# Kernel optimization log

Measured on AMD Instinct MI355X. Metric: run time of the kernel, lower is better.

Reference implementation:

```python
import math
import jax, jax.numpy as jnp
import numpy as np

B, T, C = 2, 2048, 1024
NH, D = 16, 64


def setup_inputs() -> dict:
    key = jax.random.key(0)
    k1, k2, k3, k4 = jax.random.split(key, 4)
    x = jax.random.normal(k1, (B, T, C), dtype=jnp.float32)
    W_attn = jax.random.normal(k2, (3 * C, C), dtype=jnp.float32) * 0.02
    b_attn = jnp.zeros((3 * C,), dtype=jnp.float32)
    W_proj = jax.random.normal(k3, (C, C), dtype=jnp.float32) * 0.02
    b_proj = jnp.zeros((C,), dtype=jnp.float32)
    bV = jax.random.normal(k4, (NH, D), dtype=jnp.float32) * 0.05
    return {"x": x, "W_attn": W_attn, "b_attn": b_attn,
            "W_proj": W_proj, "b_proj": b_proj, "bV": bV}


def reference(x, W_attn, b_attn, W_proj, b_proj, bV):
    Bb, Tt, Cc = x.shape
    # fused qkv projection (torch Linear: x @ W.T + b)
    qkv = x @ W_attn.T + b_attn                     # [B,T,3C]
    q, k, v = jnp.split(qkv, 3, axis=2)
    q = q.reshape(Bb, Tt, NH, D).transpose(0, 2, 1, 3)  # [B,H,T,D]
    k = k.reshape(Bb, Tt, NH, D).transpose(0, 2, 1, 3)
    v = v.reshape(Bb, Tt, NH, D).transpose(0, 2, 1, 3)
    v = v + bV[None, :, None, :]                    # V-O symmetry-breaking bias
    scores = jnp.einsum('bhqd,bhkd->bhqk', q, k) / math.sqrt(D)
    causal = jnp.tril(jnp.ones((Tt, Tt), dtype=bool))
    scores = jnp.where(causal[None, None], scores, -jnp.inf)
    att = jax.nn.softmax(scores, axis=-1)           # [B,H,T,T]
    y = jnp.einsum('bhqk,bhkd->bhqd', att, v)
    y = y.transpose(0, 2, 1, 3).reshape(Bb, Tt, Cc)
    return y @ W_proj.T + b_proj
```

## Files before the change

kernel.cpp:

```cpp
#include <hip/hip_runtime.h>

#define DEVI __device__ __forceinline__

typedef __bf16 bf16x8 __attribute__((ext_vector_type(8)));
typedef float  f32x4  __attribute__((ext_vector_type(4)));

static DEVI unsigned short f2bf(float f) {
  unsigned u = __builtin_bit_cast(unsigned, f);
  u = u + 0x7fffu + ((u >> 16) & 1u);
  return (unsigned short)(u >> 16);
}
static DEVI unsigned short f2bf_trunc(float f) {
  return (unsigned short)(__builtin_bit_cast(unsigned, f) >> 16);
}

#define EXP2F(x) __builtin_amdgcn_exp2f(x)

typedef __attribute__((address_space(3))) void* lds_vp;
typedef const __attribute__((address_space(1))) void* glob_vp;
#define GL2LDS16(g, l) __builtin_amdgcn_global_load_lds((glob_vp)(g), (lds_vp)(l), 16, 0, 0)

__global__ void __launch_bounds__(256) conv_bf16(const float* __restrict__ in,
                                                 unsigned short* __restrict__ out, int n4) {
  int i = (int)blockIdx.x * 256 + (int)threadIdx.x;
  if (i >= n4) return;
  float4 v = reinterpret_cast<const float4*>(in)[i];
  ushort4 o;
  o.x = f2bf(v.x); o.y = f2bf(v.y); o.z = f2bf(v.z); o.w = f2bf(v.w);
  reinterpret_cast<ushort4*>(out)[i] = o;
}

#define GSTAGE(t_, bufi_) do {                                                    \
    const int kk_ = (t_)*64;                                                      \
    _Pragma("unroll")                                                             \
    for (int jq = 0; jq < 4; jq++) {                                              \
      const int row_ = w*32 + jq*8 + (l >> 3);                                    \
      GL2LDS16(A  + (size_t)(r0 + row_)*K + kk_ + scol, &sA[bufi_][(w*32 + jq*8)*64]); \
      GL2LDS16(Bm + (size_t)(c0 + row_)*K + kk_ + scol, &sB[bufi_][(w*32 + jq*8)*64]); \
    } } while (0)

template<int EPI>
__global__ void __launch_bounds__(256) gemm_bt(
    const unsigned short* __restrict__ A,
    const unsigned short* __restrict__ Bm,
    const float* __restrict__ bias,
    const float* __restrict__ bV,
    unsigned short* __restrict__ outQ,
    unsigned short* __restrict__ outK,
    unsigned short* __restrict__ outVT,
    float* __restrict__ outF)
{
  constexpr int K = 1024;
  constexpr int NSTEP = 16;
  __shared__ unsigned short sA[2][128*64];
  __shared__ unsigned short sB[2][128*64];
  const int tid = (int)threadIdx.x;
  const int w = tid >> 6;
  const int l = tid & 63;
  const int l15 = l & 15, lg = l >> 4;
  const int r0 = (int)blockIdx.y * 128;
  const int c0 = (int)blockIdx.x * 128;
  const int wr = (w >> 1) * 64, wc = (w & 1) * 64;
  const int scol = ((l & 7) ^ (l >> 3)) * 8;
  const int rdsw = (l & 7) * 8;

  f32x4 acc[4][4];
#pragma unroll
  for (int i = 0; i < 4; i++)
#pragma unroll
    for (int j = 0; j < 4; j++) acc[i][j] = (f32x4){0.f, 0.f, 0.f, 0.f};

  GSTAGE(0, 0);
  GSTAGE(1, 1);
  for (int t = 0; t < NSTEP; t++) {
    if (t < NSTEP-1) asm volatile("s_waitcnt vmcnt(8)" ::: "memory");
    else             asm volatile("s_waitcnt vmcnt(0)" ::: "memory");
    __builtin_amdgcn_s_barrier();
    const int bufi = t & 1;
    bf16x8 av[2][4], bv[2][4];
#pragma unroll
    for (int ks = 0; ks < 2; ks++) {
#pragma unroll
      for (int mi = 0; mi < 4; mi++)
        av[ks][mi] = *(const bf16x8*)&sA[bufi][(wr + mi*16 + l15)*64 + ((ks*32 + lg*8) ^ rdsw)];
#pragma unroll
      for (int ni = 0; ni < 4; ni++)
        bv[ks][ni] = *(const bf16x8*)&sB[bufi][(wc + ni*16 + l15)*64 + ((ks*32 + lg*8) ^ rdsw)];
    }
    asm volatile("s_waitcnt lgkmcnt(0)" ::: "memory");
    __builtin_amdgcn_s_barrier();
    if (t + 2 < NSTEP) GSTAGE(t + 2, bufi);
#pragma unroll
    for (int ks = 0; ks < 2; ks++)
#pragma unroll
      for (int mi = 0; mi < 4; mi++)
#pragma unroll
        for (int ni = 0; ni < 4; ni++)
          acc[mi][ni] = __builtin_amdgcn_mfma_f32_16x16x32_bf16(av[ks][mi], bv[ks][ni], acc[mi][ni], 0, 0, 0);
  }

#pragma unroll
  for (int mi = 0; mi < 4; mi++) {
    const int rbase = r0 + wr + mi*16 + lg*4;
#pragma unroll
    for (int ni = 0; ni < 4; ni++) {
      const int c = c0 + wc + ni*16 + l15;
      const float bsv = bias[c];
      if constexpr (EPI == 0) {
        const int which = c >> 10;
        const int cc = c & 1023;
        const int h = cc >> 6;
        const int d = cc & 63;
        const float bvv = (which == 2) ? bV[h*64 + d] : 0.f;
#pragma unroll
        for (int i = 0; i < 4; i++) {
          const int rr = rbase + i;
          const int b = rr >> 11;
          const int t = rr & 2047;
          const int bh = b*16 + h;
          const float v = acc[mi][ni][i] + bsv;
          if (which == 0)      outQ[((size_t)bh*2048 + t)*64 + d] = f2bf(v * 0.1803368801f);
          else if (which == 1) outK[((size_t)bh*2048 + t)*64 + d] = f2bf(v);
          else                 outVT[((size_t)bh*64 + d)*2048 + t] = f2bf(v + bvv);
        }
      } else {
#pragma unroll
        for (int i = 0; i < 4; i++)
          outF[(size_t)(rbase + i)*1024 + c] = acc[mi][ni][i] + bsv;
      }
    }
  }
}

#define ASTAGE(kt_, bufi_) do {                                                   \
    _Pragma("unroll")                                                             \
    for (int jq = 0; jq < 2; jq++) {                                              \
      const int chunk_ = w*2 + jq;                                                \
      GL2LDS16(Kh + (size_t)((kt_)*64 + chunk_*8 + (l >> 3))*64 + srcsw, &sK[bufi_][chunk_*512]); \
      GL2LDS16(Vh + (size_t)(chunk_*8 + (l >> 3))*2048 + (kt_)*64 + srcsw, &sV[bufi_][chunk_*512]); \
    } } while (0)

__global__ void __launch_bounds__(256) attn_fwd(
    const unsigned short* __restrict__ Q,
    const unsigned short* __restrict__ Kc,
    const unsigned short* __restrict__ VT,
    unsigned short* __restrict__ att)
{
  __shared__ unsigned short sK[2][64*64];
  __shared__ unsigned short sV[2][64*64];
  __shared__ unsigned short sP[4][16*64];

  const int tid = (int)threadIdx.x;
  const int w = tid >> 6, l = tid & 63;
  const int l15 = l & 15, lg = l >> 4;
  const int bh = (int)blockIdx.x;
  const int qt = (int)gridDim.y - 1 - (int)blockIdx.y;
  const int qw = qt * 64 + w * 16;

  const unsigned short* Qh = Q  + (size_t)bh * (2048*64);
  const unsigned short* Kh = Kc + (size_t)bh * (2048*64);
  const unsigned short* Vh = VT + (size_t)bh * (2048*64);

  bf16x8 qf[2];
#pragma unroll
  for (int ks = 0; ks < 2; ks++)
    qf[ks] = *(const bf16x8*)&Qh[(size_t)(qw + l15)*64 + ks*32 + lg*8];

  f32x4 o[4];
#pragma unroll
  for (int nd = 0; nd < 4; nd++) o[nd] = (f32x4){0.f, 0.f, 0.f, 0.f};
  float lpart[4];
#pragma unroll
  for (int i = 0; i < 4; i++) lpart[i] = 0.f;

  const int srcsw = ((l & 7) ^ (l >> 3)) * 8;
  const int rdsw  = (l15 & 7) * 8;

  ASTAGE(0, 0);
  if (qt >= 1) ASTAGE(1, 1);
  for (int kt = 0; kt <= qt; kt++) {
    if (kt < qt) asm volatile("s_waitcnt vmcnt(4)" ::: "memory");
    else         asm volatile("s_waitcnt vmcnt(0)" ::: "memory");
    __builtin_amdgcn_s_barrier();
    const int bufi = kt & 1;
    {
      f32x4 s[4];
#pragma unroll
      for (int ni = 0; ni < 4; ni++) s[ni] = (f32x4){0.f, 0.f, 0.f, 0.f};
#pragma unroll
      for (int ks = 0; ks < 2; ks++) {
        bf16x8 kb[4];
#pragma unroll
        for (int ni = 0; ni < 4; ni++)
          kb[ni] = *(const bf16x8*)&sK[bufi][(ni*16 + l15)*64 + ((ks*32 + lg*8) ^ rdsw)];
        __builtin_amdgcn_s_setprio(1);
#pragma unroll
        for (int ni = 0; ni < 4; ni++)
          s[ni] = __builtin_amdgcn_mfma_f32_16x16x32_bf16(qf[ks], kb[ni], s[ni], 0, 0, 0);
        __builtin_amdgcn_s_setprio(0);
      }
      if (kt == qt) {
#pragma unroll
        for (int i = 0; i < 4; i++) {
          const int qq = qw + lg*4 + i;
#pragma unroll
          for (int ni = 0; ni < 4; ni++) {
            const int key = kt*64 + ni*16 + l15;
            if (key > qq) s[ni][i] = -1e30f;
          }
        }
      }
      unsigned short* pw = &sP[w][0];
#pragma unroll
      for (int i = 0; i < 4; i++) {
        float ps = 0.f;
        const int row = lg*4 + i;
        const int psw = (row & 7) << 3;
#pragma unroll
        for (int ni = 0; ni < 4; ni++) {
          const float p = EXP2F(s[ni][i]);
          ps += p;
          pw[row*64 + ((ni*16 + l15) ^ psw)] = f2bf_trunc(p);
        }
        lpart[i] += ps;
      }
#pragma unroll
      for (int ks = 0; ks < 2; ks++) {
        bf16x8 pf, vb[4];
        pf = *(const bf16x8*)&pw[l15*64 + ((ks*32 + lg*8) ^ rdsw)];
#pragma unroll
        for (int nd = 0; nd < 4; nd++)
          vb[nd] = *(const bf16x8*)&sV[bufi][(nd*16 + l15)*64 + ((ks*32 + lg*8) ^ rdsw)];
        __builtin_amdgcn_s_setprio(1);
#pragma unroll
        for (int nd = 0; nd < 4; nd++)
          o[nd] = __builtin_amdgcn_mfma_f32_16x16x32_bf16(pf, vb[nd], o[nd], 0, 0, 0);
        __builtin_amdgcn_s_setprio(0);
      }
    }
    asm volatile("s_waitcnt lgkmcnt(0)" ::: "memory");
    __builtin_amdgcn_s_barrier();
    if (kt + 2 <= qt) ASTAGE(kt + 2, bufi);
  }

  const int b = bh >> 4, h = bh & 15;
#pragma unroll
  for (int i = 0; i < 4; i++) {
    float lp = lpart[i];
    lp += __shfl_xor(lp, 1);
    lp += __shfl_xor(lp, 2);
    lp += __shfl_xor(lp, 4);
    lp += __shfl_xor(lp, 8);
    const float rinv = 1.0f / lp;
    const int qq = qw + lg*4 + i;
#pragma unroll
    for (int nd = 0; nd < 4; nd++) {
      const int d = nd*16 + l15;
      att[((size_t)(b*2048 + qq))*1024 + h*64 + d] = f2bf(o[nd][i] * rinv);
    }
  }
}

extern "C" void kernel_launch(void* const* d_in, const int* in_sizes, int n_in,
                              void* d_out, int out_size, void* d_ws, size_t ws_size,
                              hipStream_t stream) {
  const float* x      = (const float*)d_in[0];
  const float* W_attn = (const float*)d_in[1];
  const float* b_attn = (const float*)d_in[2];
  const float* W_proj = (const float*)d_in[3];
  const float* b_proj = (const float*)d_in[4];
  const float* bV     = (const float*)d_in[5];
  float* out = (float*)d_out;
  char* ws = (char*)d_ws;

  unsigned short* xb   = (unsigned short*)(ws);
  unsigned short* wab  = (unsigned short*)(ws + (8u  << 20));
  unsigned short* wpb  = (unsigned short*)(ws + (14u << 20));
  unsigned short* qb   = (unsigned short*)(ws + (16u << 20));
  unsigned short* kb   = (unsigned short*)(ws + (24u << 20));
  unsigned short* vtb  = (unsigned short*)(ws + (32u << 20));
  unsigned short* attb = (unsigned short*)(ws + (40u << 20));

  conv_bf16<<<4096, 256, 0, stream>>>(x,      xb,  1048576);
  conv_bf16<<<3072, 256, 0, stream>>>(W_attn, wab,  786432);
  conv_bf16<<<1024, 256, 0, stream>>>(W_proj, wpb,  262144);

  gemm_bt<0><<<dim3(24, 32), 256, 0, stream>>>(xb, wab, b_attn, bV, qb, kb, vtb, nullptr);
  attn_fwd<<<dim3(32, 32), 256, 0, stream>>>(qb, kb, vtb, attb);
  gemm_bt<1><<<dim3(8, 32), 256, 0, stream>>>(attb, wpb, b_proj, nullptr, nullptr, nullptr, nullptr, out);
}
```

Baseline: 122.2 us.

## Halve GEMM K-tile, repack LDS swizzle, add XCD-aware block remap and occupancy hint

The GEMM K-step shrinks from 64 to 32, which halves LDS use per block (32 KB to 16 KB) and doubles the number of pipeline steps. The LDS layout is repacked so two 32-element rows share one 64-element line with an XOR swizzle. The launch-bounds hint is raised to 5 waves per SIMD so more blocks can be resident. Block indices are also remapped so consecutive workgroups spread across the 8 XCDs, which may improve L2 locality. The cost is twice as many barriers and waitcnt round trips per K with less MFMA work between them.

```diff
diff --git a/kernel.cpp b/kernel.cpp
--- a/kernel.cpp
+++ b/kernel.cpp
@@ -31,16 +31,20 @@
 }
 
 #define GSTAGE(t_, bufi_) do {                                                    \
-    const int kk_ = (t_)*64;                                                      \
+    const int kk_ = (t_)*32;                                                      \
     _Pragma("unroll")                                                             \
-    for (int jq = 0; jq < 4; jq++) {                                              \
-      const int row_ = w*32 + jq*8 + (l >> 3);                                    \
-      GL2LDS16(A  + (size_t)(r0 + row_)*K + kk_ + scol, &sA[bufi_][(w*32 + jq*8)*64]); \
-      GL2LDS16(Bm + (size_t)(c0 + row_)*K + kk_ + scol, &sB[bufi_][(w*32 + jq*8)*64]); \
+    for (int jq = 0; jq < 2; jq++) {                                              \
+      const int ch_  = w*2 + jq;                                                  \
+      const int L_   = ch_*8 + (l >> 3);                                          \
+      const int g_   = (l & 7) ^ (L_ & 7);                                        \
+      const int row_ = L_*2 + (g_ >> 2);                                          \
+      const int cb_  = (g_ & 3)*8;                                                \
+      GL2LDS16(A  + (size_t)(r0 + row_)*K + kk_ + cb_, &sA[bufi_][ch_*512]);      \
+      GL2LDS16(Bm + (size_t)(c0 + row_)*K + kk_ + cb_, &sB[bufi_][ch_*512]);      \
     } } while (0)
 
 template<int EPI>
-__global__ void __launch_bounds__(256) gemm_bt(
+__global__ void __launch_bounds__(256, 5) gemm_bt(
     const unsigned short* __restrict__ A,
     const unsigned short* __restrict__ Bm,
     const float* __restrict__ bias,
@@ -51,18 +55,22 @@
     float* __restrict__ outF)
 {
   constexpr int K = 1024;
-  constexpr int NSTEP = 16;
-  __shared__ unsigned short sA[2][128*64];
-  __shared__ unsigned short sB[2][128*64];
+  constexpr int NSTEP = 32;
+  __shared__ unsigned short sA[2][64*64];
+  __shared__ unsigned short sB[2][64*64];
   const int tid = (int)threadIdx.x;
   const int w = tid >> 6;
   const int l = tid & 63;
   const int l15 = l & 15, lg = l >> 4;
-  const int r0 = (int)blockIdx.y * 128;
-  const int c0 = (int)blockIdx.x * 128;
+
+  const int nwg = (int)(gridDim.x * gridDim.y);
+  int lin = (int)blockIdx.y * (int)gridDim.x + (int)blockIdx.x;
+  lin = (lin & 7) * (nwg >> 3) + (lin >> 3);
+  const int bx = lin % (int)gridDim.x;
+  const int by = lin / (int)gridDim.x;
+  const int r0 = by * 128;
+  const int c0 = bx * 128;
   const int wr = (w >> 1) * 64, wc = (w & 1) * 64;
-  const int scol = ((l & 7) ^ (l >> 3)) * 8;
-  const int rdsw = (l & 7) * 8;
 
   f32x4 acc[4][4];
 #pragma unroll
@@ -73,30 +81,29 @@
   GSTAGE(0, 0);
   GSTAGE(1, 1);
   for (int t = 0; t < NSTEP; t++) {
-    if (t < NSTEP-1) asm volatile("s_waitcnt vmcnt(8)" ::: "memory");
+    if (t < NSTEP-1) asm volatile("s_waitcnt vmcnt(4)" ::: "memory");
     else             asm volatile("s_waitcnt vmcnt(0)" ::: "memory");
     __builtin_amdgcn_s_barrier();
     const int bufi = t & 1;
-    bf16x8 av[2][4], bv[2][4];
-#pragma unroll
-    for (int ks = 0; ks < 2; ks++) {
-#pragma unroll
-      for (int mi = 0; mi < 4; mi++)
-        av[ks][mi] = *(const bf16x8*)&sA[bufi][(wr + mi*16 + l15)*64 + ((ks*32 + lg*8) ^ rdsw)];
+    bf16x8 av[4], bv[4];
+#pragma unroll
+    for (int mi = 0; mi < 4; mi++) {
+      const int row = wr + mi*16 + l15;
+      av[mi] = *(const bf16x8*)&sA[bufi][(row >> 1)*64 + ((((row & 1)*4 + lg) ^ ((row >> 1) & 7))*8)];
+    }
+#pragma unroll
+    for (int ni = 0; ni < 4; ni++) {
+      const int row = wc + ni*16 + l15;
+      bv[ni] = *(const bf16x8*)&sB[bufi][(row >> 1)*64 + ((((row & 1)*4 + lg) ^ ((row >> 1) & 7))*8)];
+    }
+    asm volatile("s_waitcnt lgkmcnt(0)" ::: "memory");
+    __builtin_amdgcn_s_barrier();
+    if (t + 2 < NSTEP) GSTAGE(t + 2, bufi);
+#pragma unroll
+    for (int mi = 0; mi < 4; mi++)
 #pragma unroll
       for (int ni = 0; ni < 4; ni++)
-        bv[ks][ni] = *(const bf16x8*)&sB[bufi][(wc + ni*16 + l15)*64 + ((ks*32 + lg*8) ^ rdsw)];
-    }
-    asm volatile("s_waitcnt lgkmcnt(0)" ::: "memory");
-    __builtin_amdgcn_s_barrier();
-    if (t + 2 < NSTEP) GSTAGE(t + 2, bufi);
-#pragma unroll
-    for (int ks = 0; ks < 2; ks++)
-#pragma unroll
-      for (int mi = 0; mi < 4; mi++)
-#pragma unroll
-        for (int ni = 0; ni < 4; ni++)
-          acc[mi][ni] = __builtin_amdgcn_mfma_f32_16x16x32_bf16(av[ks][mi], bv[ks][ni], acc[mi][ni], 0, 0, 0);
+        acc[mi][ni] = __builtin_amdgcn_mfma_f32_16x16x32_bf16(av[mi], bv[ni], acc[mi][ni], 0, 0, 0);
   }
 
 #pragma unroll
```

After: 131.1 us. +7.3%, slower.

## Double attention query tile to 128 rows per block, 32 per wave

Applied to the files above, without the earlier changes.

Each attention block now handles 128 query rows, with each wave owning 32 rows as two 16-row MFMA sub-tiles. Every K/V tile staged in LDS is therefore reused by twice as many queries, halving global K/V traffic and the grid size. The cost is more registers per wave, a larger P buffer in LDS, half as many blocks (512), and waves that sit idle on the last diagonal K tile. Waves skip compute for K tiles beyond their own causal limit but still hit the barriers.

```diff
diff --git a/kernel.cpp b/kernel.cpp
--- a/kernel.cpp
+++ b/kernel.cpp
@@ -148,45 +148,55 @@
 {
   __shared__ unsigned short sK[2][64*64];
   __shared__ unsigned short sV[2][64*64];
-  __shared__ unsigned short sP[4][16*64];
+  __shared__ unsigned short sP[4][32*64];
 
   const int tid = (int)threadIdx.x;
   const int w = tid >> 6, l = tid & 63;
   const int l15 = l & 15, lg = l >> 4;
   const int bh = (int)blockIdx.x;
   const int qt = (int)gridDim.y - 1 - (int)blockIdx.y;
-  const int qw = qt * 64 + w * 16;
+  const int qw = qt * 128 + w * 32;
 
   const unsigned short* Qh = Q  + (size_t)bh * (2048*64);
   const unsigned short* Kh = Kc + (size_t)bh * (2048*64);
   const unsigned short* Vh = VT + (size_t)bh * (2048*64);
 
-  bf16x8 qf[2];
-#pragma unroll
-  for (int ks = 0; ks < 2; ks++)
-    qf[ks] = *(const bf16x8*)&Qh[(size_t)(qw + l15)*64 + ks*32 + lg*8];
-
-  f32x4 o[4];
-#pragma unroll
-  for (int nd = 0; nd < 4; nd++) o[nd] = (f32x4){0.f, 0.f, 0.f, 0.f};
-  float lpart[4];
-#pragma unroll
-  for (int i = 0; i < 4; i++) lpart[i] = 0.f;
+  bf16x8 qf[2][2];
+#pragma unroll
+  for (int mi = 0; mi < 2; mi++)
+#pragma unroll
+    for (int ks = 0; ks < 2; ks++)
+      qf[mi][ks] = *(const bf16x8*)&Qh[(size_t)(qw + mi*16 + l15)*64 + ks*32 + lg*8];
+
+  f32x4 o[2][4];
+#pragma unroll
+  for (int mi = 0; mi < 2; mi++)
+#pragma unroll
+    for (int nd = 0; nd < 4; nd++) o[mi][nd] = (f32x4){0.f, 0.f, 0.f, 0.f};
+  float lpart[2][4];
+#pragma unroll
+  for (int mi = 0; mi < 2; mi++)
+#pragma unroll
+    for (int i = 0; i < 4; i++) lpart[mi][i] = 0.f;
 
   const int srcsw = ((l & 7) ^ (l >> 3)) * 8;
   const int rdsw  = (l15 & 7) * 8;
 
+  const int ktB = 2*qt + 1;
+  const int ktW = qw >> 6;
   ASTAGE(0, 0);
-  if (qt >= 1) ASTAGE(1, 1);
-  for (int kt = 0; kt <= qt; kt++) {
-    if (kt < qt) asm volatile("s_waitcnt vmcnt(4)" ::: "memory");
-    else         asm volatile("s_waitcnt vmcnt(0)" ::: "memory");
+  ASTAGE(1, 1);
+  for (int kt = 0; kt <= ktB; kt++) {
+    if (kt < ktB) asm volatile("s_waitcnt vmcnt(4)" ::: "memory");
+    else          asm volatile("s_waitcnt vmcnt(0)" ::: "memory");
     __builtin_amdgcn_s_barrier();
     const int bufi = kt & 1;
-    {
-      f32x4 s[4];
-#pragma unroll
-      for (int ni = 0; ni < 4; ni++) s[ni] = (f32x4){0.f, 0.f, 0.f, 0.f};
+    if (kt <= ktW) {
+      f32x4 s[2][4];
+#pragma unroll
+      for (int mi = 0; mi < 2; mi++)
+#pragma unroll
+        for (int ni = 0; ni < 4; ni++) s[mi][ni] = (f32x4){0.f, 0.f, 0.f, 0.f};
 #pragma unroll
       for (int ks = 0; ks < 2; ks++) {
         bf16x8 kb[4];
@@ -195,70 +205,82 @@
           kb[ni] = *(const bf16x8*)&sK[bufi][(ni*16 + l15)*64 + ((ks*32 + lg*8) ^ rdsw)];
         __builtin_amdgcn_s_setprio(1);
 #pragma unroll
-        for (int ni = 0; ni < 4; ni++)
-          s[ni] = __builtin_amdgcn_mfma_f32_16x16x32_bf16(qf[ks], kb[ni], s[ni], 0, 0, 0);
+        for (int mi = 0; mi < 2; mi++)
+#pragma unroll
+          for (int ni = 0; ni < 4; ni++)
+            s[mi][ni] = __builtin_amdgcn_mfma_f32_16x16x32_bf16(qf[mi][ks], kb[ni], s[mi][ni], 0, 0, 0);
         __builtin_amdgcn_s_setprio(0);
       }
-      if (kt == qt) {
+      if (kt == ktW) {
+#pragma unroll
+        for (int mi = 0; mi < 2; mi++)
+#pragma unroll
+          for (int i = 0; i < 4; i++) {
+            const int qq = qw + mi*16 + lg*4 + i;
+#pragma unroll
+            for (int ni = 0; ni < 4; ni++) {
+              const int key = kt*64 + ni*16 + l15;
+              if (key > qq) s[mi][ni][i] = -1e30f;
+            }
+          }
+      }
+      unsigned short* pw = &sP[w][0];
+#pragma unroll
+      for (int mi = 0; mi < 2; mi++)
 #pragma unroll
         for (int i = 0; i < 4; i++) {
-          const int qq = qw + lg*4 + i;
+          float ps = 0.f;
+          const int row = mi*16 + lg*4 + i;
+          const int psw = (row & 7) << 3;
 #pragma unroll
           for (int ni = 0; ni < 4; ni++) {
-            const int key = kt*64 + ni*16 + l15;
-            if (key > qq) s[ni][i] = -1e30f;
+            const float p = EXP2F(s[mi][ni][i]);
+            ps += p;
+            pw[row*64 + ((ni*16 + l15) ^ psw)] = f2bf_trunc(p);
           }
+          lpart[mi][i] += ps;
         }
-      }
-      unsigned short* pw = &sP[w][0];
-#pragma unroll
-      for (int i = 0; i < 4; i++) {
-        float ps = 0.f;
-        const int row = lg*4 + i;
-        const int psw = (row & 7) << 3;
-#pragma unroll
-        for (int ni = 0; ni < 4; ni++) {
-          const float p = EXP2F(s[ni][i]);
-          ps += p;
-          pw[row*64 + ((ni*16 + l15) ^ psw)] = f2bf_trunc(p);
-        }
-        lpart[i] += ps;
-      }
 #pragma unroll
       for (int ks = 0; ks < 2; ks++) {
-        bf16x8 pf, vb[4];
-        pf = *(const bf16x8*)&pw[l15*64 + ((ks*32 + lg*8) ^ rdsw)];
+        bf16x8 pf[2], vb[4];
+#pragma unroll
+        for (int mi = 0; mi < 2; mi++)
+          pf[mi] = *(const bf16x8*)&pw[(mi*16 + l15)*64 + ((ks*32 + lg*8) ^ rdsw)];
 #pragma unroll
         for (int nd = 0; nd < 4; nd++)
           vb[nd] = *(const bf16x8*)&sV[bufi][(nd*16 + l15)*64 + ((ks*32 + lg*8) ^ rdsw)];
         __builtin_amdgcn_s_setprio(1);
 #pragma unroll
-        for (int nd = 0; nd < 4; nd++)
-          o[nd] = __builtin_amdgcn_mfma_f32_16x16x32_bf16(pf, vb[nd], o[nd], 0, 0, 0);
+        for (int mi = 0; mi < 2; mi++)
+#pragma unroll
+          for (int nd = 0; nd < 4; nd++)
+            o[mi][nd] = __builtin_amdgcn_mfma_f32_16x16x32_bf16(pf[mi], vb[nd], o[mi][nd], 0, 0, 0);
         __builtin_amdgcn_s_setprio(0);
       }
     }
     asm volatile("s_waitcnt lgkmcnt(0)" ::: "memory");
     __builtin_amdgcn_s_barrier();
-    if (kt + 2 <= qt) ASTAGE(kt + 2, bufi);
+    if (kt + 2 <= ktB) ASTAGE(kt + 2, bufi);
   }
 
   const int b = bh >> 4, h = bh & 15;
 #pragma unroll
-  for (int i = 0; i < 4; i++) {
-    float lp = lpart[i];
-    lp += __shfl_xor(lp, 1);
-    lp += __shfl_xor(lp, 2);
-    lp += __shfl_xor(lp, 4);
-    lp += __shfl_xor(lp, 8);
-    const float rinv = 1.0f / lp;
-    const int qq = qw + lg*4 + i;
-#pragma unroll
-    for (int nd = 0; nd < 4; nd++) {
-      const int d = nd*16 + l15;
-      att[((size_t)(b*2048 + qq))*1024 + h*64 + d] = f2bf(o[nd][i] * rinv);
+  for (int mi = 0; mi < 2; mi++)
+#pragma unroll
+    for (int i = 0; i < 4; i++) {
+      float lp = lpart[mi][i];
+      lp += __shfl_xor(lp, 1);
+      lp += __shfl_xor(lp, 2);
+      lp += __shfl_xor(lp, 4);
+      lp += __shfl_xor(lp, 8);
+      const float rinv = 1.0f / lp;
+      const int qq = qw + mi*16 + lg*4 + i;
+#pragma unroll
+      for (int nd = 0; nd < 4; nd++) {
+        const int d = nd*16 + l15;
+        att[((size_t)(b*2048 + qq))*1024 + h*64 + d] = f2bf(o[mi][nd][i] * rinv);
+      }
     }
-  }
 }
 
 extern "C" void kernel_launch(void* const* d_in, const int* in_sizes, int n_in,
@@ -286,6 +308,6 @@
   conv_bf16<<<1024, 256, 0, stream>>>(W_proj, wpb,  262144);
 
   gemm_bt<0><<<dim3(24, 32), 256, 0, stream>>>(xb, wab, b_attn, bV, qb, kb, vtb, nullptr);
-  attn_fwd<<<dim3(32, 32), 256, 0, stream>>>(qb, kb, vtb, attb);
+  attn_fwd<<<dim3(32, 16), 256, 0, stream>>>(qb, kb, vtb, attb);
   gemm_bt<1><<<dim3(8, 32), 256, 0, stream>>>(attb, wpb, b_proj, nullptr, nullptr, nullptr, nullptr, out);
 }
```

New measurement: 135.4 us. 1.11x slower.
